# Optimization experiments

Hardware: AMD Instinct MI355X
Metric: run time of the kernel (lower is better)

## Reference

```python
import jax, jax.numpy as jnp
import numpy as np

B, L, DIM = 8, 512, 8          # batch, seq len, raw channels (value dim D = 2*DIM = 16)
ET, HID, H = 128, 128, 2       # embed_time, hidden_size, num_heads
MAXLEN = 512
NEG = -1e9


def setup_inputs() -> dict:
    key = jax.random.key(0)
    ks = jax.random.split(key, 40)
    def n(i, shape, s=0.05):
        return jax.random.normal(ks[i], shape, jnp.float32) * s
    vals = jax.random.normal(ks[0], (B, L, DIM), jnp.float32)
    msk = (jax.random.uniform(ks[1], (B, L, DIM)) > 0.2).astype(jnp.float32)
    x = jnp.concatenate([vals, msk], -1)                      # (B, L, 2*DIM)
    time_steps = jax.random.uniform(ks[2], (B, L), jnp.float32)
    return {
        'x': x, 'time_steps': time_steps,
        # learned time embedding: Linear(1, ET-1) periodic + Linear(1,1)
        'w_per': n(3, (1, ET - 1)), 'b_per': n(4, (ET - 1,)),
        'w_lin': n(5, (1, 1)), 'b_lin': n(6, (1,)),
        # MultiTimeAttention projections
        'Wq_t': n(7, (ET, ET)), 'bq_t': n(8, (ET,)),
        'Wk_t': n(9, (ET, ET)), 'bk_t': n(10, (ET,)),
        'Wo_t': n(11, (2 * DIM * H, HID)), 'bo_t': n(12, (HID,)),
        'pos_emb': n(13, (MAXLEN + 1, HID)), 'cls_emb': n(14, (1, HID)),
        # transformer block (BERT-style post-LN encoder layer, d_ff=HID)
        'tWq': n(15, (HID, HID)), 'tbq': n(16, (HID,)),
        'tWk': n(17, (HID, HID)), 'tbk': n(18, (HID,)),
        'tWv': n(19, (HID, HID)), 'tbv': n(20, (HID,)),
        'tWo': n(21, (HID, HID)), 'tbo': n(22, (HID,)),
        'ln1_g': jnp.ones((HID,), jnp.float32), 'ln1_b': jnp.zeros((HID,), jnp.float32),
        'fW1': n(23, (HID, HID)), 'fb1': n(24, (HID,)),
        'fW2': n(25, (HID, HID)), 'fb2': n(26, (HID,)),
        'ln2_g': jnp.ones((HID,), jnp.float32), 'ln2_b': jnp.zeros((HID,), jnp.float32),
        # BertPooler
        'pW': n(27, (HID, HID)), 'pb': n(28, (HID,)),
    }


def _time_emb(tt, w_per, b_per, w_lin, b_lin):
    tt = tt[..., None]                                        # (B, L, 1)
    return jnp.concatenate([tt @ w_lin + b_lin, jnp.sin(tt @ w_per + b_per)], -1)


def _ln(x, g, b, eps=1e-5):
    m = x.mean(-1, keepdims=True)
    v = ((x - m) ** 2).mean(-1, keepdims=True)
    return (x - m) / jnp.sqrt(v + eps) * g + b


def _mta(q_emb, k_emb, value, mask, Wq, bq, Wk, bk, Wo, bo):
    # MultiTimeAttention: scores broadcast to value-channel axis, softmax over keys
    D = value.shape[-1]
    dk = ET // H
    def split(e, W, b):
        p = e @ W + b
        return p.reshape(e.shape[0], -1, H, dk).transpose(0, 2, 1, 3)
    q = split(q_emb, Wq, bq)                                  # (Bq, H, Lq, dk)
    k = split(k_emb, Wk, bk)                                  # (B,  H, Lk, dk)
    scores = jnp.matmul(q, k.swapaxes(-1, -2)) / jnp.sqrt(jnp.float32(dk))  # (B,H,Lq,Lk)
    s5 = jnp.where(mask[:, None, None, :, :] == 0, NEG, scores[..., None])  # (B,H,Lq,Lk,D)
    p = jax.nn.softmax(s5, axis=-2)
    out = jnp.einsum('bhqkd,bkd->bhqd', p, value)             # (B, H, Lq, D)
    Bv = value.shape[0]
    out = out.transpose(0, 2, 1, 3).reshape(Bv, -1, H * D)
    return out @ Wo + bo


def _tblock(x, tWq, tbq, tWk, tbk, tWv, tbv, tWo, tbo, ln1_g, ln1_b,
            fW1, fb1, fW2, fb2, ln2_g, ln2_b):
    Bq, Lq, _ = x.shape
    dk = HID // H
    def heads(W, b):
        return (x @ W + b).reshape(Bq, Lq, H, dk).transpose(0, 2, 1, 3)
    q, k, v = heads(tWq, tbq), heads(tWk, tbk), heads(tWv, tbv)
    a = jax.nn.softmax(jnp.matmul(q, k.swapaxes(-1, -2)) / jnp.sqrt(jnp.float32(dk)), -1)
    o = jnp.matmul(a, v).transpose(0, 2, 1, 3).reshape(Bq, Lq, HID) @ tWo + tbo
    x = _ln(x + o, ln1_g, ln1_b)
    f = jax.nn.relu(x @ fW1 + fb1) @ fW2 + fb2
    return _ln(x + f, ln2_g, ln2_b)


def reference(x, time_steps, w_per, b_per, w_lin, b_lin,
              Wq_t, bq_t, Wk_t, bk_t, Wo_t, bo_t, pos_emb, cls_emb,
              tWq, tbq, tWk, tbk, tWv, tbv, tWo, tbo, ln1_g, ln1_b,
              fW1, fb1, fW2, fb2, ln2_g, ln2_b, pW, pb):
    Bx = x.shape[0]
    mask_half = x[:, :, DIM:]
    mask = jnp.concatenate([mask_half, mask_half], -1)        # (B, L, 2*DIM)
    key_e = _time_emb(time_steps, w_per, b_per, w_lin, b_lin)
    tq_e = _time_emb(time_steps, w_per, b_per, w_lin, b_lin)  # query_time_steps=None -> same
    cls_t = jnp.linspace(0.0, 1.0, 128, dtype=jnp.float32)[None]
    cls_q_e = _time_emb(cls_t, w_per, b_per, w_lin, b_lin)    # (1, 128, ET)
    cls_out = _mta(cls_q_e, key_e, x, mask, Wq_t, bq_t, Wk_t, bk_t, Wo_t, bo_t)
    out = _mta(tq_e, key_e, x, mask, Wq_t, bq_t, Wk_t, bk_t, Wo_t, bo_t)
    tb = (tWq, tbq, tWk, tbk, tWv, tbv, tWo, tbo, ln1_g, ln1_b,
          fW1, fb1, fW2, fb2, ln2_g, ln2_b)
    cls_repr = jnp.broadcast_to(cls_emb[None, :, :], (Bx, 1, HID))
    # encode(cls_out, is_pooling=True), pooling='bert': no pos emb, take token 0
    h = _tblock(jnp.concatenate([cls_repr, cls_out], 1), *tb)
    cls_pooling = jnp.tanh(h[:, 0] @ pW + pb)                 # (B, HID)
    # encode(out, is_pooling=False) [pretrain path]: pos emb + transformer, drop CLS
    h2 = jnp.concatenate([cls_repr, out], 1)                  # (B, L+1, HID)
    h2 = h2 + pos_emb[:h2.shape[1]][None]
    h2 = _tblock(h2, *tb)
    last_hidden_state = h2[:, 1:]                             # (B, L, HID)
    return cls_pooling, last_hidden_state
```

## Files before the change

kernel.cpp:

```cpp
#include <hip/hip_runtime.h>
#include <hip/hip_bf16.h>
#include <math.h>


static constexpr int NM_ = 8 * 513;
static constexpr int NC_ = 8 * 129;
static constexpr int NT_ = NM_ + NC_;
static constexpr int VTS_ = 5248;

using bf = __hip_bfloat16;
typedef __attribute__((ext_vector_type(8))) short bf16x8;
typedef __attribute__((ext_vector_type(4))) short bf16x4;
typedef __attribute__((ext_vector_type(4))) float floatx4;
typedef __attribute__((ext_vector_type(8))) unsigned short ushortx8;

__device__ __forceinline__ float wave_reduce_sum(float v) {
    #pragma unroll
    for (int off = 32; off >= 1; off >>= 1) v += __shfl_xor(v, off);
    return v;
}
__device__ __forceinline__ float wave_reduce_max(float v) {
    #pragma unroll
    for (int off = 32; off >= 1; off >>= 1) v = fmaxf(v, __shfl_xor(v, off));
    return v;
}
__device__ __forceinline__ float u2f(unsigned short u) {
    return __uint_as_float(((unsigned)u) << 16);
}
__device__ __forceinline__ unsigned short f2u(float f) {
    unsigned u = __float_as_uint(f);
    return (unsigned short)((u + 0x7FFF + ((u >> 16) & 1)) >> 16);
}
__device__ __forceinline__ bf16x8 join8(bf16x4 lo, bf16x4 hi) {
    return __builtin_shufflevector(lo, hi, 0, 1, 2, 3, 4, 5, 6, 7);
}
__device__ __forceinline__ float rdin(const void* p, int i, int flag) {
    return flag ? u2f(((const unsigned short*)p)[i]) : ((const float*)p)[i];
}

struct PrepAll {
    const void* src[32]; int n[32]; int dstoff[32];
    int cstart[32]; int cnum[32];
    int ncv;
    const void* wsrc[8]; unsigned short* wdst[8]; float wscale[8];
    const void* ts; const void* w_per; const void* b_per;
    const void* w_lin; const void* b_lin;
    unsigned short* key_e16;
    unsigned short* btg;
    const void* xsrc;
    unsigned short* vt;
    const unsigned short* det;
};
__global__ void prep_all_kernel(PrepAll a, float* dst) {
    int flag = (a.det[0] == 0x3F80u) ? 1 : 0;
    int blk = blockIdx.x, tid = threadIdx.x;
    if (blk < a.ncv) {
        int which = -1, bi = 0;
        #pragma unroll
        for (int i = 0; i < 32; ++i)
            if (blk >= a.cstart[i] && blk < a.cstart[i] + a.cnum[i]) { which = i; bi = blk - a.cstart[i]; }
        if (which < 0) return;
        int i = bi * 256 + tid;
        if (i < a.n[which]) dst[a.dstoff[which] + i] = rdin(a.src[which], i, flag);
    } else if (blk < a.ncv + 512) {
        int p = blk - a.ncv;
        int m = p >> 6;
        int idx = (p & 63) * 256 + tid;
        int c = idx >> 9;
        int l = (idx >> 3) & 63;
        int j = idx & 7;
        int k = (c >> 3) * 32 + (l >> 4) * 8 + j;
        int n = (c & 7) * 16 + (l & 15);
        a.wdst[m][idx] = f2u(rdin(a.wsrc[m], k * 128 + n, flag) * a.wscale[m]);
    } else if (blk < a.ncv + 512 + 2112) {
        int p = blk - a.ncv - 512;
        int row = p * 2 + (tid >> 7), j = tid & 127;
        float t = (row < 4096) ? rdin(a.ts, row, flag)
                               : (float)(row - 4096) * (1.0f / 127.0f);
        float v;
        if (j == 0) v = t * rdin(a.w_lin, 0, flag) + rdin(a.b_lin, 0, flag);
        else        v = sinf(t * rdin(a.w_per, j - 1, flag) + rdin(a.b_per, j - 1, flag));
        a.key_e16[row * 128 + j] = f2u(v);
    } else if (blk < a.ncv + 512 + 2112 + 32) {
        int p = blk - a.ncv - 512 - 2112;
        int e0 = (p * 256 + tid) * 8;
        int b = e0 >> 13;
        int c = (e0 >> 9) & 15;
        int k0 = e0 & 511;
        unsigned short out[8];
        #pragma unroll
        for (int j = 0; j < 8; ++j) {
            int k = k0 + j;
            float m = rdin(a.xsrc, (b * 512 + k) * 16 + 8 + (c & 7), flag);
            float val = (c < 8) ? rdin(a.xsrc, (b * 512 + k) * 16 + c, flag) * m : m;
            out[j] = f2u(val);
        }
        *(ushortx8*)(a.btg + e0) = *(ushortx8*)out;
    } else {
        int p = blk - a.ncv - 512 - 2112 - 32;
        int idx = p * 256 + tid;
        int n = idx / 14, c8 = idx - n * 14;
        ushortx8 z = {0, 0, 0, 0, 0, 0, 0, 0};
        *(ushortx8*)(a.vt + (size_t)n * VTS_ + 5136 + c8 * 8) = z;
    }
}

struct GemmM {
    const void* A[3]; const unsigned short* W[3]; const float* bias[3];
    unsigned short* C[3];
    int M[3]; float bscale[3];
};
__global__ void __launch_bounds__(256)
gemm_mfma_kernel(GemmM p) {
    int y = blockIdx.y;
    const unsigned short* Wsw = p.W[y];
    const float* bias = p.bias[y];
    unsigned short* C = p.C[y];
    int M = p.M[y];
    float bscale = p.bscale[y];
    int m0 = blockIdx.x * 16;
    if (m0 >= M) return;
    int tid = threadIdx.x;
    int wv = tid >> 6, lane = tid & 63;
    int am = lane & 15, aq = lane >> 4;
    const unsigned short* A = (const unsigned short*)p.A[y];
    const unsigned short* Arow = A + (size_t)(m0 + am) * 128;
    floatx4 acc0 = {0.f, 0.f, 0.f, 0.f}, acc1 = acc0;
    #pragma unroll
    for (int ks = 0; ks < 4; ++ks) {
        bf16x8 af = *(const bf16x8*)(Arow + ks * 32 + aq * 8);
        const unsigned short* base = Wsw + ((size_t)ks * 8 + 2 * wv) * 512 + lane * 8;
        bf16x8 b0 = *(const bf16x8*)(base);
        bf16x8 b1 = *(const bf16x8*)(base + 512);
        acc0 = __builtin_amdgcn_mfma_f32_16x16x32_bf16(af, b0, acc0, 0, 0, 0);
        acc1 = __builtin_amdgcn_mfma_f32_16x16x32_bf16(af, b1, acc1, 0, 0, 0);
    }
    int col = lane & 15, rowb = (lane >> 4) * 4;
    #pragma unroll
    for (int t = 0; t < 2; ++t) {
        floatx4 acc = t ? acc1 : acc0;
        int n = wv * 32 + t * 16 + col;
        float bv = bias[n] * bscale;
        #pragma unroll
        for (int rg = 0; rg < 4; ++rg)
            C[(size_t)(m0 + rowb + rg) * 128 + n] = f2u(acc[rg] + bv);
    }
}

__global__ void __launch_bounds__(256)
mta_att_kernel(const unsigned short* qp_cls, const unsigned short* qp_main,
               const unsigned short* kp, const unsigned short* btg,
               float* att_cls, float* att_mn) {
    int is_cls = (blockIdx.x >= 32);
    int qt = is_cls ? (blockIdx.x - 32) : blockIdx.x;
    int h = blockIdx.y, b = blockIdx.z;
    int tid = threadIdx.x, lane = tid & 63, wv = tid >> 6;
    __shared__ unsigned short sp[16][520];
    __shared__ float red[1024 + 256];
    int q0 = qt * 16;
    int m = lane & 15, g = lane >> 4;

    const unsigned short* qrow = is_cls ? (qp_cls + (size_t)(q0 + m) * 128 + h * 64)
                                        : (qp_main + (size_t)(b * 512 + q0 + m) * 128 + h * 64);
    bf16x8 qf0 = *(const bf16x8*)(qrow + g * 8);
    bf16x8 qf1 = *(const bf16x8*)(qrow + 32 + g * 8);

    const unsigned short* kbase = kp + ((size_t)b * 512) * 128 + h * 64;
    #pragma unroll
    for (int kt = 0; kt < 8; ++kt) {
        int colk = kt * 64 + wv * 16 + m;
        const unsigned short* kb = kbase + (size_t)colk * 128;
        bf16x8 b0 = *(const bf16x8*)(kb + g * 8);
        bf16x8 b1 = *(const bf16x8*)(kb + 32 + g * 8);
        floatx4 acc = {0.f, 0.f, 0.f, 0.f};
        acc = __builtin_amdgcn_mfma_f32_16x16x32_bf16(qf0, b0, acc, 0, 0, 0);
        acc = __builtin_amdgcn_mfma_f32_16x16x32_bf16(qf1, b1, acc, 0, 0, 0);
        #pragma unroll
        for (int rg = 0; rg < 4; ++rg) sp[g * 4 + rg][colk] = f2u(acc[rg]);
    }
    __syncthreads();

    for (int rr = wv; rr < 16; rr += 4) {
        float mx = -1e30f;
        for (int k = lane; k < 512; k += 64) mx = fmaxf(mx, u2f(sp[rr][k]));
        mx = wave_reduce_max(mx);
        for (int k = lane; k < 512; k += 64) sp[rr][k] = f2u(expf(u2f(sp[rr][k]) - mx));
    }
    __syncthreads();

    floatx4 macc = {0.f, 0.f, 0.f, 0.f};
    {
        const unsigned short* bbase = btg + ((size_t)(b * 16 + m)) * 512 + g * 8;
        #pragma unroll
        for (int cc = 0; cc < 4; ++cc) {
            int koff = (wv + cc * 4) * 32;
            bf16x8 af = *(const bf16x8*)&sp[m][koff + g * 8];
            bf16x8 bfv = *(const bf16x8*)(bbase + koff);
            macc = __builtin_amdgcn_mfma_f32_16x16x32_bf16(af, bfv, macc, 0, 0, 0);
        }
    }
    float* redC = red;
    float* Cfull = red + 1024;
    #pragma unroll
    for (int rg = 0; rg < 4; ++rg) redC[tid * 4 + rg] = macc[rg];
    __syncthreads();
    {
        int l = tid >> 2, rg = tid & 3;
        float s = redC[l * 4 + rg] + redC[(64 + l) * 4 + rg]
                + redC[(128 + l) * 4 + rg] + redC[(192 + l) * 4 + rg];
        int row = (l >> 4) * 4 + rg, c = l & 15;
        Cfull[row * 16 + c] = s;
    }
    __syncthreads();
    if (tid < 128) {
        int r = tid >> 3, c = tid & 7;
        float num = Cfull[r * 16 + c];
        float den = Cfull[r * 16 + 8 + c];
        int row = q0 + r;
        float* dst = is_cls ? (att_cls + (size_t)(b * 128 + row) * 32)
                            : (att_mn + (size_t)(b * 512 + row) * 32);
        dst[h * 16 + c] = num / den;
        dst[h * 16 + 8 + c] = 1.0f;
    }
}

__global__ void __launch_bounds__(256)
mta_qkv_kernel(const float* att, const float* Wo, const float* bo,
               const float* cls_emb, const float* pos, float* xin,
               const unsigned short* Wq, const unsigned short* Wk, const unsigned short* Wv,
               const float* bq, const float* bk, const float* bv_,
               unsigned short* outq, unsigned short* outk, unsigned short* vT) {
    int m0 = blockIdx.x * 16;
    __shared__ float As32[16][36];
    __shared__ unsigned short As[16][136];
    int tid = threadIdx.x;
    int r = tid >> 4, g = tid & 15, c0 = g * 8;

    int R = m0 + r;
    int srow, prow;
    if (R < NM_) {
        int b = R / 513, rr = R - b * 513;
        srow = (rr == 0) ? -1 : 1024 + b * 512 + (rr - 1);
        prow = rr;
    } else {
        int mc = R - NM_;
        int b = mc / 129, rr = mc - b * 129;
        srow = (rr == 0) ? -1 : b * 128 + (rr - 1);
        prow = -1;
    }
    if (g < 2 && srow >= 0) {
        const float* src = att + (size_t)srow * 32 + g * 16;
        *(float4*)&As32[r][g * 16]      = *(const float4*)(src);
        *(float4*)&As32[r][g * 16 + 4]  = *(const float4*)(src + 4);
        *(float4*)&As32[r][g * 16 + 8]  = *(const float4*)(src + 8);
        *(float4*)&As32[r][g * 16 + 12] = *(const float4*)(src + 12);
    }
    __syncthreads();

    float acc[8];
    if (srow < 0) {
        #pragma unroll
        for (int j = 0; j < 8; ++j) acc[j] = cls_emb[c0 + j];
    } else {
        #pragma unroll
        for (int j = 0; j < 8; ++j) acc[j] = bo[c0 + j];
        #pragma unroll 8
        for (int k = 0; k < 32; ++k) {
            float a = As32[r][k];
            const float4 w0 = *(const float4*)(Wo + (size_t)k * 128 + c0);
            const float4 w1 = *(const float4*)(Wo + (size_t)k * 128 + c0 + 4);
            acc[0] = fmaf(a, w0.x, acc[0]); acc[1] = fmaf(a, w0.y, acc[1]);
            acc[2] = fmaf(a, w0.z, acc[2]); acc[3] = fmaf(a, w0.w, acc[3]);
            acc[4] = fmaf(a, w1.x, acc[4]); acc[5] = fmaf(a, w1.y, acc[5]);
            acc[6] = fmaf(a, w1.z, acc[6]); acc[7] = fmaf(a, w1.w, acc[7]);
        }
    }
    if (prow >= 0) {
        const float* pr = pos + (size_t)prow * 128 + c0;
        float4 p0 = *(const float4*)(pr);
        float4 p1 = *(const float4*)(pr + 4);
        acc[0] += p0.x; acc[1] += p0.y; acc[2] += p0.z; acc[3] += p0.w;
        acc[4] += p1.x; acc[5] += p1.y; acc[6] += p1.z; acc[7] += p1.w;
    }
    *(float4*)(xin + (size_t)R * 128 + c0) = make_float4(acc[0], acc[1], acc[2], acc[3]);
    *(float4*)(xin + (size_t)R * 128 + c0 + 4) = make_float4(acc[4], acc[5], acc[6], acc[7]);
    *(ushort4*)&As[r][c0] = make_ushort4(f2u(acc[0]), f2u(acc[1]), f2u(acc[2]), f2u(acc[3]));
    *(ushort4*)&As[r][c0 + 4] = make_ushort4(f2u(acc[4]), f2u(acc[5]), f2u(acc[6]), f2u(acc[7]));
    __syncthreads();

    int wv = tid >> 6, lane = tid & 63;
    int am = lane & 15, aq = lane >> 4;
    int col = lane & 15, rowb = (lane >> 4) * 4;
    const unsigned short* Ws[3] = {Wq, Wk, Wv};
    const float* bs[3] = {bq, bk, bv_};
    float bsc[3] = {0.125f, 1.f, 1.f};
    unsigned short* Cs[2] = {outq, outk};
    #pragma unroll
    for (int y = 0; y < 3; ++y) {
        floatx4 acc0 = {0.f, 0.f, 0.f, 0.f}, acc1 = acc0;
        #pragma unroll
        for (int ks = 0; ks < 4; ++ks) {
            bf16x8 af = *(bf16x8*)&As[am][ks * 32 + aq * 8];
            const unsigned short* base = Ws[y] + ((size_t)ks * 8 + 2 * wv) * 512 + lane * 8;
            bf16x8 b0 = *(const bf16x8*)(base);
            bf16x8 b1 = *(const bf16x8*)(base + 512);
            acc0 = __builtin_amdgcn_mfma_f32_16x16x32_bf16(af, b0, acc0, 0, 0, 0);
            acc1 = __builtin_amdgcn_mfma_f32_16x16x32_bf16(af, b1, acc1, 0, 0, 0);
        }
        #pragma unroll
        for (int t = 0; t < 2; ++t) {
            floatx4 a2 = t ? acc1 : acc0;
            int n = wv * 32 + t * 16 + col;
            float bvv = bs[y][n] * bsc[y];
            #pragma unroll
            for (int rg = 0; rg < 4; ++rg) {
                unsigned short val = f2u(a2[rg] + bvv);
                if (y < 2) Cs[y][(size_t)(m0 + rowb + rg) * 128 + n] = val;
                else       vT[(size_t)n * VTS_ + (m0 + rowb + rg)] = val;
            }
        }
    }
}

__global__ void __launch_bounds__(256)
tb_att_kernel(const unsigned short* qp, const unsigned short* kp,
              const unsigned short* vT, unsigned short* outp) {
    int is_cls = (blockIdx.x >= 33);
    int qt = is_cls ? blockIdx.x - 33 : blockIdx.x;
    int h = blockIdx.y, b = blockIdx.z;
    int Lq = is_cls ? 129 : 513;
    int base = is_cls ? (4104 + b * 129) : (b * 513);
    int nkt = is_cls ? 3 : 9;
    int tid = threadIdx.x, lane = tid & 63, wv = tid >> 6;
    __shared__ unsigned short sp[16][588];
    __shared__ float rinv[16];
    int q0 = qt * 16;
    int m = lane & 15, g = lane >> 4;

    int qr = q0 + m; if (qr >= Lq) qr = Lq - 1;
    const unsigned short* qrow = qp + (size_t)(base + qr) * 128 + h * 64;
    bf16x8 qf0 = *(const bf16x8*)(qrow + g * 8);
    bf16x8 qf1 = *(const bf16x8*)(qrow + 32 + g * 8);

    for (int kt = 0; kt < nkt; ++kt) {
        int colk = kt * 64 + wv * 16 + m;
        int krow = (colk < Lq) ? colk : (Lq - 1);
        const unsigned short* kb = kp + (size_t)(base + krow) * 128 + h * 64;
        bf16x8 b0 = *(const bf16x8*)(kb + g * 8);
        bf16x8 b1 = *(const bf16x8*)(kb + 32 + g * 8);
        floatx4 acc = {0.f, 0.f, 0.f, 0.f};
        acc = __builtin_amdgcn_mfma_f32_16x16x32_bf16(qf0, b0, acc, 0, 0, 0);
        acc = __builtin_amdgcn_mfma_f32_16x16x32_bf16(qf1, b1, acc, 0, 0, 0);
        #pragma unroll
        for (int rg = 0; rg < 4; ++rg)
            sp[g * 4 + rg][colk] = f2u((colk < Lq) ? acc[rg] : -1e30f);
    }
    __syncthreads();

    int kend = nkt * 64;
    for (int rr = wv; rr < 16; rr += 4) {
        float mx = -1e30f;
        for (int k = lane; k < kend; k += 64) mx = fmaxf(mx, u2f(sp[rr][k]));
        mx = wave_reduce_max(mx);
        float sum = 0.f;
        for (int k = lane; k < kend; k += 64) {
            float e = expf(u2f(sp[rr][k]) - mx);
            sp[rr][k] = f2u(e);
            sum += e;
        }
        sum = wave_reduce_sum(sum);
        if (lane == 0) rinv[rr] = 1.f / sum;
    }
    __syncthreads();

    floatx4 oacc = {0.f, 0.f, 0.f, 0.f};
    const unsigned short* vbase = vT + (size_t)(h * 64 + wv * 16 + m) * VTS_ + base;
    for (int kt = 0; kt < nkt; ++kt) {
        int k0 = kt * 64;
        #pragma unroll
        for (int c = 0; c < 2; ++c) {
            bf16x4 plo = *(const bf16x4*)&sp[m][k0 + c * 32 + g * 8];
            bf16x4 phi = *(const bf16x4*)&sp[m][k0 + c * 32 + g * 8 + 4];
            bf16x8 vf = *(const bf16x8*)(vbase + k0 + c * 32 + g * 8);
            oacc = __builtin_amdgcn_mfma_f32_16x16x32_bf16(join8(plo, phi), vf, oacc, 0, 0, 0);
        }
    }
    int dcol = wv * 16 + m;
    #pragma unroll
    for (int rg = 0; rg < 4; ++rg) {
        int q = g * 4 + rg;
        int qout = q0 + q;
        if (qout < Lq)
            outp[(size_t)(base + qout) * 128 + h * 64 + dcol] = f2u(oacc[rg] * rinv[q]);
    }
}

__global__ void __launch_bounds__(256)
attnout_ffn_kernel(const unsigned short* A, const unsigned short* Wao, const float* bao,
                   const float* resid, const float* g1, const float* b1ln,
                   const unsigned short* W1, const float* fb1,
                   const unsigned short* W2, const float* fb2,
                   const float* g2, const float* b2ln,
                   const float* pW, const float* pb, float* dout) {
    int m0 = blockIdx.x * 16;
    __shared__ unsigned short As[16][136];
    __shared__ float Xs[16][128];
    __shared__ unsigned short Hs[16][136];
    __shared__ float redS[4][4][4], redQ[4][4][4];
    __shared__ float smean[16], sinv[16];
    __shared__ float x2row[128];
    __shared__ int poolb;
    int tid = threadIdx.x;
    if (tid == 0) poolb = -1;
    {
        int r = tid >> 4, c0 = (tid & 15) * 8;
        *(ushortx8*)&As[r][c0] = *(const ushortx8*)(A + (size_t)(m0 + r) * 128 + c0);
    }
    __syncthreads();

    int wv = tid >> 6, lane = tid & 63;
    int am = lane & 15, aq = lane >> 4;
    int col = lane & 15, g = lane >> 4, rowb = g * 4;

    float ov[2][4];
    {
        floatx4 acc0 = {0.f, 0.f, 0.f, 0.f}, acc1 = acc0;
        #pragma unroll
        for (int ks = 0; ks < 4; ++ks) {
            bf16x8 af = *(bf16x8*)&As[am][ks * 32 + aq * 8];
            const unsigned short* base = Wao + ((size_t)ks * 8 + 2 * wv) * 512 + lane * 8;
            bf16x8 bb0 = *(const bf16x8*)(base);
            bf16x8 bb1 = *(const bf16x8*)(base + 512);
            acc0 = __builtin_amdgcn_mfma_f32_16x16x32_bf16(af, bb0, acc0, 0, 0, 0);
            acc1 = __builtin_amdgcn_mfma_f32_16x16x32_bf16(af, bb1, acc1, 0, 0, 0);
        }
        #pragma unroll
        for (int t = 0; t < 2; ++t) {
            int n = wv * 32 + t * 16 + col;
            float bv = bao[n];
            floatx4 acc = t ? acc1 : acc0;
            #pragma unroll
            for (int rg = 0; rg < 4; ++rg)
                ov[t][rg] = acc[rg] + bv + resid[(size_t)(m0 + rowb + rg) * 128 + n];
        }
    }
    #pragma unroll
    for (int rg = 0; rg < 4; ++rg) {
        float s = ov[0][rg] + ov[1][rg];
        float q = ov[0][rg] * ov[0][rg] + ov[1][rg] * ov[1][rg];
        #pragma unroll
        for (int off = 8; off >= 1; off >>= 1) {
            s += __shfl_xor(s, off);
            q += __shfl_xor(q, off);
        }
        if ((lane & 15) == 0) { redS[wv][g][rg] = s; redQ[wv][g][rg] = q; }
    }
    __syncthreads();
    if (tid < 16) {
        int gg = tid >> 2, rg = tid & 3;
        float s = redS[0][gg][rg] + redS[1][gg][rg] + redS[2][gg][rg] + redS[3][gg][rg];
        float q = redQ[0][gg][rg] + redQ[1][gg][rg] + redQ[2][gg][rg] + redQ[3][gg][rg];
        float mean = s * 0.0078125f;
        float var = q * 0.0078125f - mean * mean;
        smean[tid] = mean;
        sinv[tid] = rsqrtf(var + 1e-5f);
    }
    __syncthreads();
    #pragma unroll
    for (int t = 0; t < 2; ++t) {
        int n = wv * 32 + t * 16 + col;
        float gm = g1[n], bb = b1ln[n];
        #pragma unroll
        for (int rg = 0; rg < 4; ++rg) {
            int row = rowb + rg;
            float val = (ov[t][rg] - smean[row]) * sinv[row] * gm + bb;
            Xs[row][n] = val;
            As[row][n] = f2u(val);
        }
    }
    __syncthreads();

    {
        floatx4 acc0 = {0.f, 0.f, 0.f, 0.f}, acc1 = acc0;
        #pragma unroll
        for (int ks = 0; ks < 4; ++ks) {
            bf16x8 af = *(bf16x8*)&As[am][ks * 32 + aq * 8];
            const unsigned short* base = W1 + ((size_t)ks * 8 + 2 * wv) * 512 + lane * 8;
            bf16x8 bb0 = *(const bf16x8*)(base);
            bf16x8 bb1 = *(const bf16x8*)(base + 512);
            acc0 = __builtin_amdgcn_mfma_f32_16x16x32_bf16(af, bb0, acc0, 0, 0, 0);
            acc1 = __builtin_amdgcn_mfma_f32_16x16x32_bf16(af, bb1, acc1, 0, 0, 0);
        }
        #pragma unroll
        for (int t = 0; t < 2; ++t) {
            int n = wv * 32 + t * 16 + col;
            float bv = fb1[n];
            floatx4 acc = t ? acc1 : acc0;
            #pragma unroll
            for (int rg = 0; rg < 4; ++rg)
                Hs[rowb + rg][n] = f2u(fmaxf(acc[rg] + bv, 0.f));
        }
    }
    __syncthreads();

    floatx4 acc0 = {0.f, 0.f, 0.f, 0.f}, acc1 = acc0;
    #pragma unroll
    for (int ks = 0; ks < 4; ++ks) {
        bf16x8 af = *(bf16x8*)&Hs[am][ks * 32 + aq * 8];
        const unsigned short* base = W2 + ((size_t)ks * 8 + 2 * wv) * 512 + lane * 8;
        bf16x8 bb0 = *(const bf16x8*)(base);
        bf16x8 bb1 = *(const bf16x8*)(base + 512);
        acc0 = __builtin_amdgcn_mfma_f32_16x16x32_bf16(af, bb0, acc0, 0, 0, 0);
        acc1 = __builtin_amdgcn_mfma_f32_16x16x32_bf16(af, bb1, acc1, 0, 0, 0);
    }
    #pragma unroll
    for (int t = 0; t < 2; ++t) {
        int n = wv * 32 + t * 16 + col;
        float bv = fb2[n];
        floatx4 acc = t ? acc1 : acc0;
        #pragma unroll
        for (int rg = 0; rg < 4; ++rg)
            ov[t][rg] = acc[rg] + bv + Xs[rowb + rg][n];
    }
    #pragma unroll
    for (int rg = 0; rg < 4; ++rg) {
        float s = ov[0][rg] + ov[1][rg];
        float q = ov[0][rg] * ov[0][rg] + ov[1][rg] * ov[1][rg];
        #pragma unroll
        for (int off = 8; off >= 1; off >>= 1) {
            s += __shfl_xor(s, off);
            q += __shfl_xor(q, off);
        }
        if ((lane & 15) == 0) { redS[wv][g][rg] = s; redQ[wv][g][rg] = q; }
    }
    __syncthreads();
    if (tid < 16) {
        int gg = tid >> 2, rg = tid & 3;
        float s = redS[0][gg][rg] + redS[1][gg][rg] + redS[2][gg][rg] + redS[3][gg][rg];
        float q = redQ[0][gg][rg] + redQ[1][gg][rg] + redQ[2][gg][rg] + redQ[3][gg][rg];
        float mean = s * 0.0078125f;
        float var = q * 0.0078125f - mean * mean;
        smean[tid] = mean;
        sinv[tid] = rsqrtf(var + 1e-5f);
    }
    __syncthreads();
    #pragma unroll
    for (int t = 0; t < 2; ++t) {
        int n = wv * 32 + t * 16 + col;
        float gm = g2[n], bb = b2ln[n];
        #pragma unroll
        for (int rg = 0; rg < 4; ++rg) {
            int row = rowb + rg;
            int m = m0 + row;
            float val = (ov[t][rg] - smean[row]) * sinv[row] * gm + bb;
            if (m < NM_) {
                int b = m / 513, r = m - b * 513;
                if (r >= 1)
                    dout[1024 + (size_t)b * 65536 + (size_t)(r - 1) * 128 + n] = val;
            } else {
                int mc = m - NM_;
                int b = mc / 129, r = mc - b * 129;
                if (r == 0) {
                    x2row[n] = val;
                    if (n == 0) poolb = b;
                }
            }
        }
    }
    __syncthreads();
    if (poolb >= 0 && tid < 128) {
        float acc = pb[tid];
        for (int k = 0; k < 128; ++k) acc = fmaf(x2row[k], pW[(size_t)k * 128 + tid], acc);
        dout[(size_t)poolb * 128 + tid] = tanhf(acc);
    }
}

extern "C" void kernel_launch(void* const* d_in, const int* in_sizes, int n_in,
                              void* d_out, int out_size, void* d_ws, size_t ws_size,
                              hipStream_t stream) {
    float* w = (float*)d_ws;
    size_t off = 0;
    auto alloc = [&](size_t n) {
        float* p = w + off;
        off += (n + 3) & ~(size_t)3;
        return p;
    };
    auto allocU = [&](size_t n) { return (unsigned short*)alloc((n + 1) / 2); };

    PrepAll pa{};
    int nn = n_in < 32 ? n_in : 32;
    float* fin[32];
    const int needconv[32] = {0,0,0,0,0,0, 0,1, 0,1, 1,1, 1,1, 0,1, 0,1, 0,1,
                              0,1, 1,1, 0,1, 0,1, 1,1, 1,1};
    int ncv = 0;
    for (int i = 0; i < nn; ++i) {
        pa.src[i] = d_in[i];
        pa.n[i] = in_sizes[i];
        fin[i] = alloc(in_sizes[i]);
        pa.dstoff[i] = (int)(fin[i] - w);
        if (needconv[i]) {
            int nb = (in_sizes[i] + 255) / 256;
            pa.cstart[i] = ncv;
            pa.cnum[i] = nb;
            ncv += nb;
        } else { pa.cstart[i] = -1; pa.cnum[i] = 0; }
    }
    for (int i = nn; i < 32; ++i) {
        pa.src[i] = nullptr; pa.n[i] = 0; pa.dstoff[i] = 0;
        pa.cstart[i] = -1; pa.cnum[i] = 0;
    }
    pa.ncv = ncv;

    const float* bq_t    = fin[7];
    const float* bk_t    = fin[9];
    const float* Wo_t    = fin[10]; const float* bo_t = fin[11];
    const float* pos_emb = fin[12]; const float* cls_emb = fin[13];
    const float* tbq = fin[15]; const float* tbk = fin[17]; const float* tbv = fin[19];
    const float* tbo = fin[21];
    const float* ln1_g = fin[22]; const float* ln1_b = fin[23];
    const float* fb1 = fin[25]; const float* fb2 = fin[27];
    const float* ln2_g = fin[28]; const float* ln2_b = fin[29];
    const float* pW = fin[30]; const float* pb = fin[31];

    const int widx[8] = {8, 6, 14, 16, 18, 20, 24, 26};
    unsigned short* wsw[8];
    for (int i = 0; i < 8; ++i) {
        wsw[i] = allocU(16384);
        pa.wsrc[i] = d_in[widx[i]];
        pa.wdst[i] = wsw[i];
        pa.wscale[i] = (i == 1 || i == 2) ? 0.125f : 1.0f;
    }
    pa.ts = d_in[1]; pa.w_per = d_in[2]; pa.b_per = d_in[3];
    pa.w_lin = d_in[4]; pa.b_lin = d_in[5];
    pa.xsrc = d_in[0];
    pa.det = (const unsigned short*)d_in[22];

    unsigned short* key_e16 = allocU(4224 * 128);
    unsigned short* cls_e16 = key_e16 + 4096 * 128;
    pa.key_e16 = key_e16;
    unsigned short* btg = allocU(8 * 16 * 512);
    pa.btg = btg;

    unsigned short* qp_main16 = allocU(4096 * 128);
    unsigned short* kp_main16 = allocU(4096 * 128);
    unsigned short* qp_cls16  = allocU(128 * 128);
    float* att_all = alloc(5120 * 32);
    float* att_cls = att_all;
    float* att_mn  = att_all + 1024 * 32;
    float* xin     = alloc((size_t)NT_ * 128);
    unsigned short* tbq16 = allocU((size_t)NT_ * 128);
    unsigned short* tbk16 = allocU((size_t)NT_ * 128);
    unsigned short* vT    = allocU((size_t)128 * VTS_);
    unsigned short* tba16 = allocU((size_t)NT_ * 128);
    pa.vt = vT;
    (void)ws_size;

    float* outf = (float*)d_out;

    prep_all_kernel<<<ncv + 512 + 2112 + 32 + 7, 256, 0, stream>>>(pa, w);

    {
        GemmM p{};
        p.A[0] = key_e16; p.W[0] = wsw[0]; p.bias[0] = bk_t; p.C[0] = kp_main16;
        p.M[0] = 4096; p.bscale[0] = 1.f;
        p.A[1] = key_e16; p.W[1] = wsw[1]; p.bias[1] = bq_t; p.C[1] = qp_main16;
        p.M[1] = 4096; p.bscale[1] = 0.125f;
        p.A[2] = cls_e16; p.W[2] = wsw[1]; p.bias[2] = bq_t; p.C[2] = qp_cls16;
        p.M[2] = 128; p.bscale[2] = 0.125f;
        gemm_mfma_kernel<<<dim3(256, 3), 256, 0, stream>>>(p);
    }

    mta_att_kernel<<<dim3(40, 2, 8), 256, 0, stream>>>(qp_cls16, qp_main16, kp_main16,
                                                       btg, att_cls, att_mn);

    mta_qkv_kernel<<<321, 256, 0, stream>>>(att_all, Wo_t, bo_t, cls_emb, pos_emb, xin,
                                            wsw[2], wsw[3], wsw[4], tbq, tbk, tbv,
                                            tbq16, tbk16, vT);

    tb_att_kernel<<<dim3(42, 2, 8), 256, 0, stream>>>(tbq16, tbk16, vT, tba16);

    attnout_ffn_kernel<<<321, 256, 0, stream>>>(tba16, wsw[5], tbo, xin, ln1_g, ln1_b,
                                                wsw[6], fb1, wsw[7], fb2, ln2_g, ln2_b,
                                                pW, pb, outf);
}
```

Baseline: 188.2 us.

## Fuse MTA attention with QKV projection and transformer attention with FFN

Merges the time-attention kernel into the following Wo/QKV projection kernel, and the transformer attention kernel into the attention-output/FFN/LayerNorm kernel. Each block now loops over both heads and keeps the attention output in shared memory, so the intermediate att and tba buffers and two launches go away. Shared memory is reused through unions. The cost is fewer, longer-running blocks: 321 instead of 640, and 336 instead of 672. Head-level parallelism is serialized inside each block.

```diff
diff --git a/kernel.cpp b/kernel.cpp
--- a/kernel.cpp
+++ b/kernel.cpp
@@ -99,9 +99,11 @@
     } else {
         int p = blk - a.ncv - 512 - 2112 - 32;
         int idx = p * 256 + tid;
-        int n = idx / 14, c8 = idx - n * 14;
-        ushortx8 z = {0, 0, 0, 0, 0, 0, 0, 0};
-        *(ushortx8*)(a.vt + (size_t)n * VTS_ + 5136 + c8 * 8) = z;
+        if (idx < 128 * 14) {
+            int n = idx / 14, c8 = idx - n * 14;
+            ushortx8 z = {0, 0, 0, 0, 0, 0, 0, 0};
+            *(ushortx8*)(a.vt + (size_t)n * VTS_ + 5136 + c8 * 8) = z;
+        }
     }
 }
 
@@ -147,118 +149,111 @@
     }
 }
 
+struct MaU_att { unsigned short sp[16][520]; float red[1280]; };
+struct MaU_qkv { unsigned short As[16][136]; };
+union MaU { MaU_att att; MaU_qkv qkv; };
+
 __global__ void __launch_bounds__(256)
-mta_att_kernel(const unsigned short* qp_cls, const unsigned short* qp_main,
-               const unsigned short* kp, const unsigned short* btg,
-               float* att_cls, float* att_mn) {
-    int is_cls = (blockIdx.x >= 32);
-    int qt = is_cls ? (blockIdx.x - 32) : blockIdx.x;
-    int h = blockIdx.y, b = blockIdx.z;
-    int tid = threadIdx.x, lane = tid & 63, wv = tid >> 6;
-    __shared__ unsigned short sp[16][520];
-    __shared__ float red[1024 + 256];
+mta_fused_kernel(const unsigned short* qp_cls, const unsigned short* qp_main,
+                 const unsigned short* kp, const unsigned short* btg,
+                 const float* Wo, const float* bo, const float* cls_emb, const float* pos,
+                 float* xin,
+                 const unsigned short* Wq, const unsigned short* Wk, const unsigned short* Wv,
+                 const float* bq, const float* bk, const float* bv_,
+                 unsigned short* outq, unsigned short* outk, unsigned short* vT) {
+    __shared__ MaU U;
+    __shared__ float As32[16][36];
+    int vb = blockIdx.x, tid = threadIdx.x;
+    int lane = tid & 63, wv = tid >> 6;
+    int m = lane & 15, g = lane >> 4;
+    bool special = (vb == 320);
+    int is_cls = 0, qt = 0, b = 0;
+    if (!special) {
+        if (vb < 256) { b = vb >> 5; qt = vb & 31; }
+        else { int t = vb - 256; b = t >> 3; qt = t & 7; is_cls = 1; }
+    }
     int q0 = qt * 16;
-    int m = lane & 15, g = lane >> 4;
-
-    const unsigned short* qrow = is_cls ? (qp_cls + (size_t)(q0 + m) * 128 + h * 64)
-                                        : (qp_main + (size_t)(b * 512 + q0 + m) * 128 + h * 64);
-    bf16x8 qf0 = *(const bf16x8*)(qrow + g * 8);
-    bf16x8 qf1 = *(const bf16x8*)(qrow + 32 + g * 8);
-
-    const unsigned short* kbase = kp + ((size_t)b * 512) * 128 + h * 64;
-    #pragma unroll
-    for (int kt = 0; kt < 8; ++kt) {
-        int colk = kt * 64 + wv * 16 + m;
-        const unsigned short* kb = kbase + (size_t)colk * 128;
-        bf16x8 b0 = *(const bf16x8*)(kb + g * 8);
-        bf16x8 b1 = *(const bf16x8*)(kb + 32 + g * 8);
-        floatx4 acc = {0.f, 0.f, 0.f, 0.f};
-        acc = __builtin_amdgcn_mfma_f32_16x16x32_bf16(qf0, b0, acc, 0, 0, 0);
-        acc = __builtin_amdgcn_mfma_f32_16x16x32_bf16(qf1, b1, acc, 0, 0, 0);
-        #pragma unroll
-        for (int rg = 0; rg < 4; ++rg) sp[g * 4 + rg][colk] = f2u(acc[rg]);
-    }
-    __syncthreads();
-
-    for (int rr = wv; rr < 16; rr += 4) {
-        float mx = -1e30f;
-        for (int k = lane; k < 512; k += 64) mx = fmaxf(mx, u2f(sp[rr][k]));
-        mx = wave_reduce_max(mx);
-        for (int k = lane; k < 512; k += 64) sp[rr][k] = f2u(expf(u2f(sp[rr][k]) - mx));
-    }
-    __syncthreads();
-
-    floatx4 macc = {0.f, 0.f, 0.f, 0.f};
-    {
-        const unsigned short* bbase = btg + ((size_t)(b * 16 + m)) * 512 + g * 8;
-        #pragma unroll
-        for (int cc = 0; cc < 4; ++cc) {
-            int koff = (wv + cc * 4) * 32;
-            bf16x8 af = *(const bf16x8*)&sp[m][koff + g * 8];
-            bf16x8 bfv = *(const bf16x8*)(bbase + koff);
-            macc = __builtin_amdgcn_mfma_f32_16x16x32_bf16(af, bfv, macc, 0, 0, 0);
-        }
-    }
-    float* redC = red;
-    float* Cfull = red + 1024;
-    #pragma unroll
-    for (int rg = 0; rg < 4; ++rg) redC[tid * 4 + rg] = macc[rg];
-    __syncthreads();
-    {
-        int l = tid >> 2, rg = tid & 3;
-        float s = redC[l * 4 + rg] + redC[(64 + l) * 4 + rg]
-                + redC[(128 + l) * 4 + rg] + redC[(192 + l) * 4 + rg];
-        int row = (l >> 4) * 4 + rg, c = l & 15;
-        Cfull[row * 16 + c] = s;
-    }
-    __syncthreads();
-    if (tid < 128) {
-        int r = tid >> 3, c = tid & 7;
-        float num = Cfull[r * 16 + c];
-        float den = Cfull[r * 16 + 8 + c];
-        int row = q0 + r;
-        float* dst = is_cls ? (att_cls + (size_t)(b * 128 + row) * 32)
-                            : (att_mn + (size_t)(b * 512 + row) * 32);
-        dst[h * 16 + c] = num / den;
-        dst[h * 16 + 8 + c] = 1.0f;
-    }
-}
-
-__global__ void __launch_bounds__(256)
-mta_qkv_kernel(const float* att, const float* Wo, const float* bo,
-               const float* cls_emb, const float* pos, float* xin,
-               const unsigned short* Wq, const unsigned short* Wk, const unsigned short* Wv,
-               const float* bq, const float* bk, const float* bv_,
-               unsigned short* outq, unsigned short* outk, unsigned short* vT) {
-    int m0 = blockIdx.x * 16;
-    __shared__ float As32[16][36];
-    __shared__ unsigned short As[16][136];
-    int tid = threadIdx.x;
-    int r = tid >> 4, g = tid & 15, c0 = g * 8;
-
-    int R = m0 + r;
-    int srow, prow;
-    if (R < NM_) {
-        int b = R / 513, rr = R - b * 513;
-        srow = (rr == 0) ? -1 : 1024 + b * 512 + (rr - 1);
-        prow = rr;
-    } else {
-        int mc = R - NM_;
-        int b = mc / 129, rr = mc - b * 129;
-        srow = (rr == 0) ? -1 : b * 128 + (rr - 1);
-        prow = -1;
-    }
-    if (g < 2 && srow >= 0) {
-        const float* src = att + (size_t)srow * 32 + g * 16;
-        *(float4*)&As32[r][g * 16]      = *(const float4*)(src);
-        *(float4*)&As32[r][g * 16 + 4]  = *(const float4*)(src + 4);
-        *(float4*)&As32[r][g * 16 + 8]  = *(const float4*)(src + 8);
-        *(float4*)&As32[r][g * 16 + 12] = *(const float4*)(src + 12);
-    }
-    __syncthreads();
+
+    if (!special) {
+        for (int h = 0; h < 2; ++h) {
+            const unsigned short* qrow = is_cls
+                ? (qp_cls + (size_t)(q0 + m) * 128 + h * 64)
+                : (qp_main + (size_t)(b * 512 + q0 + m) * 128 + h * 64);
+            bf16x8 qf0 = *(const bf16x8*)(qrow + g * 8);
+            bf16x8 qf1 = *(const bf16x8*)(qrow + 32 + g * 8);
+
+            const unsigned short* kbase = kp + ((size_t)b * 512) * 128 + h * 64;
+            #pragma unroll
+            for (int kt = 0; kt < 8; ++kt) {
+                int colk = kt * 64 + wv * 16 + m;
+                const unsigned short* kb = kbase + (size_t)colk * 128;
+                bf16x8 b0 = *(const bf16x8*)(kb + g * 8);
+                bf16x8 b1 = *(const bf16x8*)(kb + 32 + g * 8);
+                floatx4 acc = {0.f, 0.f, 0.f, 0.f};
+                acc = __builtin_amdgcn_mfma_f32_16x16x32_bf16(qf0, b0, acc, 0, 0, 0);
+                acc = __builtin_amdgcn_mfma_f32_16x16x32_bf16(qf1, b1, acc, 0, 0, 0);
+                #pragma unroll
+                for (int rg = 0; rg < 4; ++rg) U.att.sp[g * 4 + rg][colk] = f2u(acc[rg]);
+            }
+            __syncthreads();
+
+            for (int rr = wv; rr < 16; rr += 4) {
+                float mx = -1e30f;
+                for (int k = lane; k < 512; k += 64) mx = fmaxf(mx, u2f(U.att.sp[rr][k]));
+                mx = wave_reduce_max(mx);
+                for (int k = lane; k < 512; k += 64)
+                    U.att.sp[rr][k] = f2u(expf(u2f(U.att.sp[rr][k]) - mx));
+            }
+            __syncthreads();
+
+            floatx4 macc = {0.f, 0.f, 0.f, 0.f};
+            {
+                const unsigned short* bbase = btg + ((size_t)(b * 16 + m)) * 512 + g * 8;
+                #pragma unroll
+                for (int cc = 0; cc < 4; ++cc) {
+                    int koff = (wv + cc * 4) * 32;
+                    bf16x8 af = *(const bf16x8*)&U.att.sp[m][koff + g * 8];
+                    bf16x8 bfv = *(const bf16x8*)(bbase + koff);
+                    macc = __builtin_amdgcn_mfma_f32_16x16x32_bf16(af, bfv, macc, 0, 0, 0);
+                }
+            }
+            float* redC = U.att.red;
+            float* Cfull = U.att.red + 1024;
+            #pragma unroll
+            for (int rg = 0; rg < 4; ++rg) redC[tid * 4 + rg] = macc[rg];
+            __syncthreads();
+            {
+                int l = tid >> 2, rg = tid & 3;
+                float s = redC[l * 4 + rg] + redC[(64 + l) * 4 + rg]
+                        + redC[(128 + l) * 4 + rg] + redC[(192 + l) * 4 + rg];
+                int row = (l >> 4) * 4 + rg, c = l & 15;
+                Cfull[row * 16 + c] = s;
+            }
+            __syncthreads();
+            if (tid < 128) {
+                int r = tid >> 3, c = tid & 7;
+                float num = Cfull[r * 16 + c];
+                float den = Cfull[r * 16 + 8 + c];
+                As32[r][h * 16 + c] = num / den;
+                As32[r][h * 16 + 8 + c] = 1.0f;
+            }
+            __syncthreads();
+        }
+    }
+
+    int r = tid >> 4, gi = tid & 15, c0 = gi * 8;
+    int segbase = is_cls ? (NM_ + b * 129) : (b * 513);
+    auto Rof = [&](int rr) -> int {
+        if (special) return (rr < 8) ? rr * 513 : NM_ + (rr - 8) * 129;
+        return segbase + 1 + q0 + rr;
+    };
+    int R = Rof(r);
+    int prow;
+    if (special) prow = (r < 8) ? 0 : -1;
+    else prow = is_cls ? -1 : (1 + q0 + r);
 
     float acc[8];
-    if (srow < 0) {
+    if (special) {
         #pragma unroll
         for (int j = 0; j < 8; ++j) acc[j] = cls_emb[c0 + j];
     } else {
@@ -284,11 +279,10 @@
     }
     *(float4*)(xin + (size_t)R * 128 + c0) = make_float4(acc[0], acc[1], acc[2], acc[3]);
     *(float4*)(xin + (size_t)R * 128 + c0 + 4) = make_float4(acc[4], acc[5], acc[6], acc[7]);
-    *(ushort4*)&As[r][c0] = make_ushort4(f2u(acc[0]), f2u(acc[1]), f2u(acc[2]), f2u(acc[3]));
-    *(ushort4*)&As[r][c0 + 4] = make_ushort4(f2u(acc[4]), f2u(acc[5]), f2u(acc[6]), f2u(acc[7]));
-    __syncthreads();
-
-    int wv = tid >> 6, lane = tid & 63;
+    *(ushort4*)&U.qkv.As[r][c0] = make_ushort4(f2u(acc[0]), f2u(acc[1]), f2u(acc[2]), f2u(acc[3]));
+    *(ushort4*)&U.qkv.As[r][c0 + 4] = make_ushort4(f2u(acc[4]), f2u(acc[5]), f2u(acc[6]), f2u(acc[7]));
+    __syncthreads();
+
     int am = lane & 15, aq = lane >> 4;
     int col = lane & 15, rowb = (lane >> 4) * 4;
     const unsigned short* Ws[3] = {Wq, Wk, Wv};
@@ -300,7 +294,7 @@
         floatx4 acc0 = {0.f, 0.f, 0.f, 0.f}, acc1 = acc0;
         #pragma unroll
         for (int ks = 0; ks < 4; ++ks) {
-            bf16x8 af = *(bf16x8*)&As[am][ks * 32 + aq * 8];
+            bf16x8 af = *(bf16x8*)&U.qkv.As[am][ks * 32 + aq * 8];
             const unsigned short* base = Ws[y] + ((size_t)ks * 8 + 2 * wv) * 512 + lane * 8;
             bf16x8 b0 = *(const bf16x8*)(base);
             bf16x8 b1 = *(const bf16x8*)(base + 512);
@@ -315,112 +309,103 @@
             #pragma unroll
             for (int rg = 0; rg < 4; ++rg) {
                 unsigned short val = f2u(a2[rg] + bvv);
-                if (y < 2) Cs[y][(size_t)(m0 + rowb + rg) * 128 + n] = val;
-                else       vT[(size_t)n * VTS_ + (m0 + rowb + rg)] = val;
-            }
-        }
-    }
-}
+                int R2 = Rof(rowb + rg);
+                if (y < 2) Cs[y][(size_t)R2 * 128 + n] = val;
+                else       vT[(size_t)n * VTS_ + R2] = val;
+            }
+        }
+    }
+}
+
+struct TbU_att { unsigned short sp[16][588]; };
+struct TbU_ffn { float Xs[16][128]; unsigned short Hs[16][136]; };
+union TbU { TbU_att att; TbU_ffn ffn; };
 
 __global__ void __launch_bounds__(256)
-tb_att_kernel(const unsigned short* qp, const unsigned short* kp,
-              const unsigned short* vT, unsigned short* outp) {
-    int is_cls = (blockIdx.x >= 33);
-    int qt = is_cls ? blockIdx.x - 33 : blockIdx.x;
-    int h = blockIdx.y, b = blockIdx.z;
+tb_fused_kernel(const unsigned short* qp, const unsigned short* kp,
+                const unsigned short* vT, const float* resid,
+                const unsigned short* Wao, const float* bao,
+                const float* g1, const float* b1ln,
+                const unsigned short* W1, const float* fb1,
+                const unsigned short* W2, const float* fb2,
+                const float* g2, const float* b2ln,
+                const float* pW, const float* pb, float* dout) {
+    __shared__ TbU U;
+    __shared__ unsigned short As[16][136];
+    __shared__ float rinv[16];
+    __shared__ float redS[4][4][4], redQ[4][4][4], smean[16], sinv[16], x2row[128];
+    __shared__ int poolb;
+
+    int xx = blockIdx.x, b = blockIdx.y, tid = threadIdx.x;
+    int is_cls = (xx >= 33);
+    int qt = is_cls ? xx - 33 : xx;
     int Lq = is_cls ? 129 : 513;
-    int base = is_cls ? (4104 + b * 129) : (b * 513);
+    int base = is_cls ? (NM_ + b * 129) : (b * 513);
     int nkt = is_cls ? 3 : 9;
-    int tid = threadIdx.x, lane = tid & 63, wv = tid >> 6;
-    __shared__ unsigned short sp[16][588];
-    __shared__ float rinv[16];
-    int q0 = qt * 16;
-    int m = lane & 15, g = lane >> 4;
-
-    int qr = q0 + m; if (qr >= Lq) qr = Lq - 1;
-    const unsigned short* qrow = qp + (size_t)(base + qr) * 128 + h * 64;
-    bf16x8 qf0 = *(const bf16x8*)(qrow + g * 8);
-    bf16x8 qf1 = *(const bf16x8*)(qrow + 32 + g * 8);
-
-    for (int kt = 0; kt < nkt; ++kt) {
-        int colk = kt * 64 + wv * 16 + m;
-        int krow = (colk < Lq) ? colk : (Lq - 1);
-        const unsigned short* kb = kp + (size_t)(base + krow) * 128 + h * 64;
-        bf16x8 b0 = *(const bf16x8*)(kb + g * 8);
-        bf16x8 b1 = *(const bf16x8*)(kb + 32 + g * 8);
-        floatx4 acc = {0.f, 0.f, 0.f, 0.f};
-        acc = __builtin_amdgcn_mfma_f32_16x16x32_bf16(qf0, b0, acc, 0, 0, 0);
-        acc = __builtin_amdgcn_mfma_f32_16x16x32_bf16(qf1, b1, acc, 0, 0, 0);
-        #pragma unroll
-        for (int rg = 0; rg < 4; ++rg)
-            sp[g * 4 + rg][colk] = f2u((colk < Lq) ? acc[rg] : -1e30f);
-    }
-    __syncthreads();
-
-    int kend = nkt * 64;
-    for (int rr = wv; rr < 16; rr += 4) {
-        float mx = -1e30f;
-        for (int k = lane; k < kend; k += 64) mx = fmaxf(mx, u2f(sp[rr][k]));
-        mx = wave_reduce_max(mx);
-        float sum = 0.f;
-        for (int k = lane; k < kend; k += 64) {
-            float e = expf(u2f(sp[rr][k]) - mx);
-            sp[rr][k] = f2u(e);
-            sum += e;
-        }
-        sum = wave_reduce_sum(sum);
-        if (lane == 0) rinv[rr] = 1.f / sum;
-    }
-    __syncthreads();
-
-    floatx4 oacc = {0.f, 0.f, 0.f, 0.f};
-    const unsigned short* vbase = vT + (size_t)(h * 64 + wv * 16 + m) * VTS_ + base;
-    for (int kt = 0; kt < nkt; ++kt) {
-        int k0 = kt * 64;
-        #pragma unroll
-        for (int c = 0; c < 2; ++c) {
-            bf16x4 plo = *(const bf16x4*)&sp[m][k0 + c * 32 + g * 8];
-            bf16x4 phi = *(const bf16x4*)&sp[m][k0 + c * 32 + g * 8 + 4];
-            bf16x8 vf = *(const bf16x8*)(vbase + k0 + c * 32 + g * 8);
-            oacc = __builtin_amdgcn_mfma_f32_16x16x32_bf16(join8(plo, phi), vf, oacc, 0, 0, 0);
-        }
-    }
-    int dcol = wv * 16 + m;
-    #pragma unroll
-    for (int rg = 0; rg < 4; ++rg) {
-        int q = g * 4 + rg;
-        int qout = q0 + q;
-        if (qout < Lq)
-            outp[(size_t)(base + qout) * 128 + h * 64 + dcol] = f2u(oacc[rg] * rinv[q]);
-    }
-}
-
-__global__ void __launch_bounds__(256)
-attnout_ffn_kernel(const unsigned short* A, const unsigned short* Wao, const float* bao,
-                   const float* resid, const float* g1, const float* b1ln,
-                   const unsigned short* W1, const float* fb1,
-                   const unsigned short* W2, const float* fb2,
-                   const float* g2, const float* b2ln,
-                   const float* pW, const float* pb, float* dout) {
-    int m0 = blockIdx.x * 16;
-    __shared__ unsigned short As[16][136];
-    __shared__ float Xs[16][128];
-    __shared__ unsigned short Hs[16][136];
-    __shared__ float redS[4][4][4], redQ[4][4][4];
-    __shared__ float smean[16], sinv[16];
-    __shared__ float x2row[128];
-    __shared__ int poolb;
-    int tid = threadIdx.x;
+    int lane = tid & 63, wv = tid >> 6;
+    int q0 = qt * 16, m = lane & 15, g = lane >> 4;
     if (tid == 0) poolb = -1;
-    {
-        int r = tid >> 4, c0 = (tid & 15) * 8;
-        *(ushortx8*)&As[r][c0] = *(const ushortx8*)(A + (size_t)(m0 + r) * 128 + c0);
-    }
-    __syncthreads();
-
-    int wv = tid >> 6, lane = tid & 63;
+
+    for (int h = 0; h < 2; ++h) {
+        int qr = q0 + m; if (qr >= Lq) qr = Lq - 1;
+        const unsigned short* qrow = qp + (size_t)(base + qr) * 128 + h * 64;
+        bf16x8 qf0 = *(const bf16x8*)(qrow + g * 8);
+        bf16x8 qf1 = *(const bf16x8*)(qrow + 32 + g * 8);
+
+        for (int kt = 0; kt < nkt; ++kt) {
+            int colk = kt * 64 + wv * 16 + m;
+            int krow = (colk < Lq) ? colk : (Lq - 1);
+            const unsigned short* kb = kp + (size_t)(base + krow) * 128 + h * 64;
+            bf16x8 b0 = *(const bf16x8*)(kb + g * 8);
+            bf16x8 b1 = *(const bf16x8*)(kb + 32 + g * 8);
+            floatx4 acc = {0.f, 0.f, 0.f, 0.f};
+            acc = __builtin_amdgcn_mfma_f32_16x16x32_bf16(qf0, b0, acc, 0, 0, 0);
+            acc = __builtin_amdgcn_mfma_f32_16x16x32_bf16(qf1, b1, acc, 0, 0, 0);
+            #pragma unroll
+            for (int rg = 0; rg < 4; ++rg)
+                U.att.sp[g * 4 + rg][colk] = f2u((colk < Lq) ? acc[rg] : -1e30f);
+        }
+        __syncthreads();
+
+        int kend = nkt * 64;
+        for (int rr = wv; rr < 16; rr += 4) {
+            float mx = -1e30f;
+            for (int k = lane; k < kend; k += 64) mx = fmaxf(mx, u2f(U.att.sp[rr][k]));
+            mx = wave_reduce_max(mx);
+            float sum = 0.f;
+            for (int k = lane; k < kend; k += 64) {
+                float e = expf(u2f(U.att.sp[rr][k]) - mx);
+                U.att.sp[rr][k] = f2u(e);
+                sum += e;
+            }
+            sum = wave_reduce_sum(sum);
+            if (lane == 0) rinv[rr] = 1.f / sum;
+        }
+        __syncthreads();
+
+        floatx4 oacc = {0.f, 0.f, 0.f, 0.f};
+        const unsigned short* vbase = vT + (size_t)(h * 64 + wv * 16 + m) * VTS_ + base;
+        for (int kt = 0; kt < nkt; ++kt) {
+            int k0 = kt * 64;
+            #pragma unroll
+            for (int c = 0; c < 2; ++c) {
+                bf16x4 plo = *(const bf16x4*)&U.att.sp[m][k0 + c * 32 + g * 8];
+                bf16x4 phi = *(const bf16x4*)&U.att.sp[m][k0 + c * 32 + g * 8 + 4];
+                bf16x8 vf = *(const bf16x8*)(vbase + k0 + c * 32 + g * 8);
+                oacc = __builtin_amdgcn_mfma_f32_16x16x32_bf16(join8(plo, phi), vf, oacc, 0, 0, 0);
+            }
+        }
+        int dcol = wv * 16 + m;
+        #pragma unroll
+        for (int rg = 0; rg < 4; ++rg) {
+            int q = g * 4 + rg;
+            As[q][h * 64 + dcol] = f2u(oacc[rg] * rinv[q]);
+        }
+        __syncthreads();
+    }
+
     int am = lane & 15, aq = lane >> 4;
-    int col = lane & 15, g = lane >> 4, rowb = g * 4;
+    int col = lane & 15, rowb = g * 4;
 
     float ov[2][4];
     {
@@ -428,9 +413,9 @@
         #pragma unroll
         for (int ks = 0; ks < 4; ++ks) {
             bf16x8 af = *(bf16x8*)&As[am][ks * 32 + aq * 8];
-            const unsigned short* base = Wao + ((size_t)ks * 8 + 2 * wv) * 512 + lane * 8;
-            bf16x8 bb0 = *(const bf16x8*)(base);
-            bf16x8 bb1 = *(const bf16x8*)(base + 512);
+            const unsigned short* wb = Wao + ((size_t)ks * 8 + 2 * wv) * 512 + lane * 8;
+            bf16x8 bb0 = *(const bf16x8*)(wb);
+            bf16x8 bb1 = *(const bf16x8*)(wb + 512);
             acc0 = __builtin_amdgcn_mfma_f32_16x16x32_bf16(af, bb0, acc0, 0, 0, 0);
             acc1 = __builtin_amdgcn_mfma_f32_16x16x32_bf16(af, bb1, acc1, 0, 0, 0);
         }
@@ -440,8 +425,11 @@
             float bv = bao[n];
             floatx4 acc = t ? acc1 : acc0;
             #pragma unroll
-            for (int rg = 0; rg < 4; ++rg)
-                ov[t][rg] = acc[rg] + bv + resid[(size_t)(m0 + rowb + rg) * 128 + n];
+            for (int rg = 0; rg < 4; ++rg) {
+                int qo = q0 + rowb + rg;
+                int rc = (qo < Lq) ? qo : (Lq - 1);
+                ov[t][rg] = acc[rg] + bv + resid[(size_t)(base + rc) * 128 + n];
+            }
         }
     }
     #pragma unroll
@@ -474,7 +462,7 @@
         for (int rg = 0; rg < 4; ++rg) {
             int row = rowb + rg;
             float val = (ov[t][rg] - smean[row]) * sinv[row] * gm + bb;
-            Xs[row][n] = val;
+            U.ffn.Xs[row][n] = val;
             As[row][n] = f2u(val);
         }
     }
@@ -485,9 +473,9 @@
         #pragma unroll
         for (int ks = 0; ks < 4; ++ks) {
             bf16x8 af = *(bf16x8*)&As[am][ks * 32 + aq * 8];
-            const unsigned short* base = W1 + ((size_t)ks * 8 + 2 * wv) * 512 + lane * 8;
-            bf16x8 bb0 = *(const bf16x8*)(base);
-            bf16x8 bb1 = *(const bf16x8*)(base + 512);
+            const unsigned short* wb = W1 + ((size_t)ks * 8 + 2 * wv) * 512 + lane * 8;
+            bf16x8 bb0 = *(const bf16x8*)(wb);
+            bf16x8 bb1 = *(const bf16x8*)(wb + 512);
             acc0 = __builtin_amdgcn_mfma_f32_16x16x32_bf16(af, bb0, acc0, 0, 0, 0);
             acc1 = __builtin_amdgcn_mfma_f32_16x16x32_bf16(af, bb1, acc1, 0, 0, 0);
         }
@@ -498,7 +486,7 @@
             floatx4 acc = t ? acc1 : acc0;
             #pragma unroll
             for (int rg = 0; rg < 4; ++rg)
-                Hs[rowb + rg][n] = f2u(fmaxf(acc[rg] + bv, 0.f));
+                U.ffn.Hs[rowb + rg][n] = f2u(fmaxf(acc[rg] + bv, 0.f));
         }
     }
     __syncthreads();
@@ -506,10 +494,10 @@
     floatx4 acc0 = {0.f, 0.f, 0.f, 0.f}, acc1 = acc0;
     #pragma unroll
     for (int ks = 0; ks < 4; ++ks) {
-        bf16x8 af = *(bf16x8*)&Hs[am][ks * 32 + aq * 8];
-        const unsigned short* base = W2 + ((size_t)ks * 8 + 2 * wv) * 512 + lane * 8;
-        bf16x8 bb0 = *(const bf16x8*)(base);
-        bf16x8 bb1 = *(const bf16x8*)(base + 512);
+        bf16x8 af = *(bf16x8*)&U.ffn.Hs[am][ks * 32 + aq * 8];
+        const unsigned short* wb = W2 + ((size_t)ks * 8 + 2 * wv) * 512 + lane * 8;
+        bf16x8 bb0 = *(const bf16x8*)(wb);
+        bf16x8 bb1 = *(const bf16x8*)(wb + 512);
         acc0 = __builtin_amdgcn_mfma_f32_16x16x32_bf16(af, bb0, acc0, 0, 0, 0);
         acc1 = __builtin_amdgcn_mfma_f32_16x16x32_bf16(af, bb1, acc1, 0, 0, 0);
     }
@@ -520,7 +508,7 @@
         floatx4 acc = t ? acc1 : acc0;
         #pragma unroll
         for (int rg = 0; rg < 4; ++rg)
-            ov[t][rg] = acc[rg] + bv + Xs[rowb + rg][n];
+            ov[t][rg] = acc[rg] + bv + U.ffn.Xs[rowb + rg][n];
     }
     #pragma unroll
     for (int rg = 0; rg < 4; ++rg) {
@@ -551,16 +539,13 @@
         #pragma unroll
         for (int rg = 0; rg < 4; ++rg) {
             int row = rowb + rg;
-            int m = m0 + row;
+            int qout = q0 + row;
             float val = (ov[t][rg] - smean[row]) * sinv[row] * gm + bb;
-            if (m < NM_) {
-                int b = m / 513, r = m - b * 513;
-                if (r >= 1)
-                    dout[1024 + (size_t)b * 65536 + (size_t)(r - 1) * 128 + n] = val;
+            if (!is_cls) {
+                if (qout >= 1 && qout < Lq)
+                    dout[1024 + (size_t)b * 65536 + (size_t)(qout - 1) * 128 + n] = val;
             } else {
-                int mc = m - NM_;
-                int b = mc / 129, r = mc - b * 129;
-                if (r == 0) {
+                if (qout == 0) {
                     x2row[n] = val;
                     if (n == 0) poolb = b;
                 }
@@ -644,20 +629,17 @@
     unsigned short* qp_main16 = allocU(4096 * 128);
     unsigned short* kp_main16 = allocU(4096 * 128);
     unsigned short* qp_cls16  = allocU(128 * 128);
-    float* att_all = alloc(5120 * 32);
-    float* att_cls = att_all;
-    float* att_mn  = att_all + 1024 * 32;
     float* xin     = alloc((size_t)NT_ * 128);
     unsigned short* tbq16 = allocU((size_t)NT_ * 128);
     unsigned short* tbk16 = allocU((size_t)NT_ * 128);
     unsigned short* vT    = allocU((size_t)128 * VTS_);
-    unsigned short* tba16 = allocU((size_t)NT_ * 128);
     pa.vt = vT;
     (void)ws_size;
 
     float* outf = (float*)d_out;
-
-    prep_all_kernel<<<ncv + 512 + 2112 + 32 + 7, 256, 0, stream>>>(pa, w);
+    int prep_nblk = ncv + 512 + 2112 + 32 + 7;
+
+    prep_all_kernel<<<prep_nblk, 256, 0, stream>>>(pa, w);
 
     {
         GemmM p{};
@@ -670,16 +652,13 @@
         gemm_mfma_kernel<<<dim3(256, 3), 256, 0, stream>>>(p);
     }
 
-    mta_att_kernel<<<dim3(40, 2, 8), 256, 0, stream>>>(qp_cls16, qp_main16, kp_main16,
-                                                       btg, att_cls, att_mn);
-
-    mta_qkv_kernel<<<321, 256, 0, stream>>>(att_all, Wo_t, bo_t, cls_emb, pos_emb, xin,
-                                            wsw[2], wsw[3], wsw[4], tbq, tbk, tbv,
-                                            tbq16, tbk16, vT);
-
-    tb_att_kernel<<<dim3(42, 2, 8), 256, 0, stream>>>(tbq16, tbk16, vT, tba16);
-
-    attnout_ffn_kernel<<<321, 256, 0, stream>>>(tba16, wsw[5], tbo, xin, ln1_g, ln1_b,
-                                                wsw[6], fb1, wsw[7], fb2, ln2_g, ln2_b,
-                                                pW, pb, outf);
-}
+    mta_fused_kernel<<<321, 256, 0, stream>>>(qp_cls16, qp_main16, kp_main16, btg,
+                                              Wo_t, bo_t, cls_emb, pos_emb, xin,
+                                              wsw[2], wsw[3], wsw[4], tbq, tbk, tbv,
+                                              tbq16, tbk16, vT);
+
+    tb_fused_kernel<<<dim3(42, 8), 256, 0, stream>>>(tbq16, tbk16, vT, xin,
+                                                     wsw[5], tbo, ln1_g, ln1_b,
+                                                     wsw[6], fb1, wsw[7], fb2,
+                                                     ln2_g, ln2_b, pW, pb, outf);
+}
```

New measurement: 207.3 us. 10.2% more time.
